# Kernel optimization log

Hardware: AMD Instinct MI355X
Metric: run time of the kernel (lower is better)

## Reference

```python
import jax, jax.numpy as jnp
import numpy as np

NUM_EXPERTS = 8
D_MODEL = 2048
D_FF = 4096
TOP_K = 2
NUM_TOKENS = 4096


def setup_inputs() -> dict:
    key = jax.random.key(0)
    k1, k2, k3, k4, k5, k6 = jax.random.split(key, 6)
    hidden_states = jax.random.normal(k1, (NUM_TOKENS, D_MODEL), dtype=jnp.float32)
    top_k_index = jax.random.randint(k2, (NUM_TOKENS, TOP_K), 0, NUM_EXPERTS)
    raw = jax.random.uniform(k3, (NUM_TOKENS, TOP_K), dtype=jnp.float32)
    top_k_weights = raw / jnp.sum(raw, axis=-1, keepdims=True)  # normalized router weights
    scale = 0.02
    Wg = jax.random.normal(k4, (NUM_EXPERTS, D_MODEL, D_FF), dtype=jnp.float32) * scale
    Wu = jax.random.normal(k5, (NUM_EXPERTS, D_MODEL, D_FF), dtype=jnp.float32) * scale
    Wd = jax.random.normal(k6, (NUM_EXPERTS, D_FF, D_MODEL), dtype=jnp.float32) * scale
    return {
        "hidden_states": hidden_states,
        "top_k_index": top_k_index,
        "top_k_weights": top_k_weights,
        "Wg": Wg,
        "Wu": Wu,
        "Wd": Wd,
    }


def reference(hidden_states, top_k_index, top_k_weights, Wg, Wu, Wd):
    T, D = hidden_states.shape
    E = Wg.shape[0]
    # Combine weights: [T, E], summing duplicate expert hits exactly as the
    # original loop's repeated index_add_ would.
    combine = jnp.zeros((T, E), dtype=top_k_weights.dtype)
    combine = combine.at[jnp.arange(T)[:, None], top_k_index].add(top_k_weights)
    # Dense all-experts SwiGLU (same math per token/expert as the gather loop)
    gate = jnp.einsum("td,edf->tef", hidden_states, Wg)   # [T, E, F]
    up = jnp.einsum("td,edf->tef", hidden_states, Wu)     # [T, E, F]
    h = jax.nn.silu(gate) * up                              # [T, E, F]
    expert_out = jnp.einsum("tef,efd->ted", h, Wd)          # [T, E, D]
    # Weighted scatter-combine
    final = jnp.einsum("ted,te->td", expert_out, combine)   # [T, D]
    return final
```

## Files before the change

kernel.cpp:

```cpp
#include <hip/hip_runtime.h>
#include <hip/hip_bf16.h>

#define NTOK 4096
#define DM   2048
#define DF   4096
#define NEXP 8
#define NPAD 10240
#define NPTILE 40

typedef __attribute__((ext_vector_type(4))) float f32x4;
typedef __attribute__((ext_vector_type(8))) short s16x8;
typedef __attribute__((ext_vector_type(2))) int   i32x2;

__device__ __forceinline__ unsigned short f2bf(float f) {
  union { float f; unsigned u; } x; x.f = f;
  unsigned r = x.u + 0x7fffu + ((x.u >> 16) & 1u);
  return (unsigned short)(r >> 16);
}
__device__ __forceinline__ unsigned pack2(float lo, float hi) {
  __hip_bfloat162 h2 = __float22bfloat162_rn(make_float2(lo, hi));
  return *reinterpret_cast<unsigned*>(&h2);
}
__device__ __forceinline__ int swz(int row, int ks) {
  return row * 32 + ((ks ^ ((row >> 1) & 3)) << 3);
}
__device__ __forceinline__ void g2l16(const void* g, void* l) {
  __builtin_amdgcn_global_load_lds(
      (const __attribute__((address_space(1))) void*)g,
      (__attribute__((address_space(3))) void*)l, 16, 0, 0);
}

#define BARRIER() asm volatile("s_barrier" ::: "memory")
#define WAITV(n)  asm volatile("s_waitcnt vmcnt(" #n ")" ::: "memory")

__global__ void k_zero_out(float* out) {
  int gid = blockIdx.x * 256 + threadIdx.x;
  *(f32x4*)(out + (size_t)gid * 4) = f32x4{0.f, 0.f, 0.f, 0.f};
}

__global__ void k_init(int* tokrow, int* counts, int* cursor) {
  int i = blockIdx.x * 256 + threadIdx.x;
  if (i < NPAD) tokrow[i] = 0;
  if (i < NEXP) { counts[i] = 0; cursor[i] = 0; }
}

__global__ void k_count(const int* __restrict__ idx, int* counts) {
  int t = blockIdx.x * 256 + threadIdx.x;
  if (t >= NTOK) return;
  int e0 = idx[2 * t], e1 = idx[2 * t + 1];
  atomicAdd(&counts[e0], 1);
  if (e1 != e0) atomicAdd(&counts[e1], 1);
}

__global__ void k_scan(const int* __restrict__ counts, int* poff) {
  if (threadIdx.x == 0) {
    int s = 0;
    for (int e = 0; e < NEXP; e++) {
      poff[e] = s;
      s += ((counts[e] + 255) & ~255);
    }
  }
}

__global__ void k_fill(const int* __restrict__ idx, const float* __restrict__ wts,
                       const int* __restrict__ poff, int* cursor,
                       int* tokrow, float* wrow) {
  int t = blockIdx.x * 256 + threadIdx.x;
  if (t >= NTOK) return;
  int e0 = idx[2 * t], e1 = idx[2 * t + 1];
  float w0 = wts[2 * t], w1 = wts[2 * t + 1];
  if (e0 == e1) {
    int g = poff[e0] + atomicAdd(&cursor[e0], 1);
    tokrow[g] = t; wrow[g] = w0 + w1;
  } else {
    int g0 = poff[e0] + atomicAdd(&cursor[e0], 1);
    tokrow[g0] = t; wrow[g0] = w0;
    int g1 = poff[e1] + atomicAdd(&cursor[e1], 1);
    tokrow[g1] = t; wrow[g1] = w1;
  }
}

__global__ void k_convX(const float* __restrict__ X, const int* __restrict__ tokrow,
                        short* __restrict__ Xg) {
  const int kt = blockIdx.x, tile = blockIdx.y, tid = threadIdx.x;
  const int part = tid & 7;
  short* dst = Xg + (size_t)(tile * 64 + kt) * 8192;
  #pragma unroll
  for (int it = 0; it < 8; it++) {
    int row = it * 32 + (tid >> 3);
    int tok = tokrow[tile * 256 + row];
    f32x4 v = *(const f32x4*)(X + (size_t)tok * DM + kt * 32 + part * 4);
    i32x2 p;
    p[0] = (int)pack2(v[0], v[1]);
    p[1] = (int)pack2(v[2], v[3]);
    int idx = row * 32 + (((part >> 1) ^ ((row >> 1) & 3)) << 3) + (part & 1) * 4;
    *(i32x2*)&dst[idx] = p;
  }
}

__global__ void k_convW(const float* __restrict__ W, short* __restrict__ dst,
                        int N, int K) {
  const int nt = blockIdx.x, kt = blockIdx.y, e = blockIdx.z;
  const int t = threadIdx.x;
  const int kg = t >> 5, nb = t & 31;
  const float* src = W + (size_t)e * K * N + (size_t)(kt * 32 + kg * 4) * N
                     + nt * 128 + nb * 4;
  f32x4 b0 = *(const f32x4*)(src);
  f32x4 b1 = *(const f32x4*)(src + N);
  f32x4 b2 = *(const f32x4*)(src + 2 * (size_t)N);
  f32x4 b3 = *(const f32x4*)(src + 3 * (size_t)N);
  short* img = dst + ((size_t)(e * (N / 128) + nt) * (K / 32) + kt) * 4096;
  const int c0 = kg >> 1, klo = (kg & 1) * 4;
  #pragma unroll
  for (int j = 0; j < 4; j++) {
    int nl = nb * 4 + j;
    i32x2 v;
    v[0] = (int)pack2(b0[j], b1[j]);
    v[1] = (int)pack2(b2[j], b3[j]);
    *(i32x2*)&img[nl * 32 + ((c0 ^ ((nl >> 1) & 3)) << 3) + klo] = v;
  }
}

__global__ __launch_bounds__(512, 2) void gemm1_kernel(
    const short* __restrict__ Xg, const short* __restrict__ Wgt,
    const short* __restrict__ Wut, const int* __restrict__ counts,
    const int* __restrict__ poff, unsigned short* __restrict__ Hs) {
  const int e = blockIdx.z;
  const int cnt = counts[e];
  const int m0 = blockIdx.y * 256;
  if (m0 >= cnt) return;
  const int nt = blockIdx.x, n0 = nt * 128;
  const int tileIdx = (poff[e] >> 8) + blockIdx.y;

  __shared__ __attribute__((aligned(16))) short As[4][8192];
  __shared__ __attribute__((aligned(16))) short Bs[4][2][4096];

  const int tid = threadIdx.x, wave = tid >> 6, lane = tid & 63;
  const int wm = wave >> 1, wn = wave & 1;
  const int lr = lane & 15, ks = lane >> 4;

  const short* aSrc = Xg + (size_t)tileIdx * 64 * 8192 + wave * 1024 + lane * 8;
  const short* gSrc = Wgt + (size_t)(e * 32 + nt) * 64 * 4096 + wave * 512 + lane * 8;
  const short* uSrc = Wut + (size_t)(e * 32 + nt) * 64 * 4096 + wave * 512 + lane * 8;

  f32x4 accg[4][4], accu[4][4];
  #pragma unroll
  for (int i = 0; i < 4; i++)
    #pragma unroll
    for (int j = 0; j < 4; j++) {
      accg[i][j] = f32x4{0.f, 0.f, 0.f, 0.f};
      accu[i][j] = f32x4{0.f, 0.f, 0.f, 0.f};
    }

  auto stage = [&](int s, int kt) {
    g2l16(aSrc + (size_t)kt * 8192,       &As[s][wave * 1024]);
    g2l16(aSrc + (size_t)kt * 8192 + 512, &As[s][wave * 1024 + 512]);
    g2l16(gSrc + (size_t)kt * 4096,       &Bs[s][0][wave * 512]);
    g2l16(uSrc + (size_t)kt * 4096,       &Bs[s][1][wave * 512]);
  };

  const int nK = DM / 32;
  stage(0, 0); stage(1, 1); stage(2, 2);
  asm volatile("s_waitcnt vmcnt(8) lgkmcnt(0)" ::: "memory");
  BARRIER();

  for (int kt = 0; kt < nK; ++kt) {
    const int s = kt & 3;
    if (kt + 3 < nK) stage((kt + 3) & 3, kt + 3);
    s16x8 af[4], bg[4], bu[4];
    #pragma unroll
    for (int mi = 0; mi < 4; mi++)
      af[mi] = *(const s16x8*)&As[s][swz(wm * 64 + mi * 16 + lr, ks)];
    #pragma unroll
    for (int ni = 0; ni < 4; ni++) {
      bg[ni] = *(const s16x8*)&Bs[s][0][swz(wn * 64 + ni * 16 + lr, ks)];
      bu[ni] = *(const s16x8*)&Bs[s][1][swz(wn * 64 + ni * 16 + lr, ks)];
    }
    __builtin_amdgcn_s_setprio(1);
    #pragma unroll
    for (int mi = 0; mi < 4; mi++)
      #pragma unroll
      for (int ni = 0; ni < 4; ni++) {
        accg[mi][ni] = __builtin_amdgcn_mfma_f32_16x16x32_bf16(af[mi], bg[ni], accg[mi][ni], 0, 0, 0);
        accu[mi][ni] = __builtin_amdgcn_mfma_f32_16x16x32_bf16(af[mi], bu[ni], accu[mi][ni], 0, 0, 0);
      }
    __builtin_amdgcn_s_setprio(0);
    if (kt + 1 < nK) {
      if (kt + 3 < nK)      { WAITV(8); }
      else if (kt + 2 < nK) { WAITV(4); }
      else                  { WAITV(0); }
      BARRIER();
    }
  }

  const size_t tb = (size_t)tileIdx * 128 * 8192;
  #pragma unroll
  for (int mi = 0; mi < 4; mi++) {
    #pragma unroll
    for (int r = 0; r < 4; r++) {
      int row = wm * 64 + mi * 16 + ks * 4 + r;
      if (m0 + row < cnt) {
        #pragma unroll
        for (int ni = 0; ni < 4; ni++) {
          int col = n0 + wn * 64 + ni * 16 + lr;
          float g = accg[mi][ni][r], u = accu[mi][ni][r];
          float sv = g / (1.f + __expf(-g));
          int ktH = col >> 5, kl = col & 31;
          Hs[tb + (size_t)ktH * 8192 + row * 32 +
             (((kl >> 3) ^ ((row >> 1) & 3)) << 3) + (kl & 7)] = f2bf(sv * u);
        }
      }
    }
  }
}

__global__ __launch_bounds__(256, 2) void gemm2_kernel(
    const unsigned short* __restrict__ Hs, const short* __restrict__ Wdt,
    const int* __restrict__ counts, const int* __restrict__ poff,
    const int* __restrict__ tokrow, const float* __restrict__ wrow,
    float* __restrict__ out) {
  const int e = blockIdx.z;
  const int cnt = counts[e];
  const int m0 = blockIdx.y * 128;
  if (m0 >= cnt) return;
  const int nt = blockIdx.x, n0 = nt * 256;
  const int tileIdx = (poff[e] >> 8) + (m0 >> 8);
  const int half = (m0 >> 7) & 1;

  __shared__ __attribute__((aligned(16))) short As[2][4096];
  __shared__ __attribute__((aligned(16))) short Bs[2][2][4096];
  __shared__ float wl[128];
  __shared__ int   tl[128];

  const int tid = threadIdx.x, wave = tid >> 6, lane = tid & 63;
  const int wm = wave >> 1, wn = wave & 1;
  const int lr = lane & 15, ks = lane >> 4;

  if (tid < 128) {
    int rp = poff[e] + m0 + tid;
    wl[tid] = wrow[rp];
    tl[tid] = tokrow[rp];
  }

  const unsigned short* aSrc = Hs + (size_t)tileIdx * 128 * 8192 + half * 4096
                               + wave * 1024 + lane * 8;
  const short* b0Src = Wdt + (size_t)(e * 16 + 2 * nt) * 128 * 4096
                       + wave * 1024 + lane * 8;
  const short* b1Src = Wdt + (size_t)(e * 16 + 2 * nt + 1) * 128 * 4096
                       + wave * 1024 + lane * 8;

  f32x4 acc0[4][4], acc1[4][4];
  #pragma unroll
  for (int i = 0; i < 4; i++)
    #pragma unroll
    for (int j = 0; j < 4; j++) {
      acc0[i][j] = f32x4{0.f, 0.f, 0.f, 0.f};
      acc1[i][j] = f32x4{0.f, 0.f, 0.f, 0.f};
    }

  auto stage = [&](int b, int kt) {
    g2l16(aSrc + (size_t)kt * 8192,        &As[b][wave * 1024]);
    g2l16(aSrc + (size_t)kt * 8192 + 512,  &As[b][wave * 1024 + 512]);
    g2l16(b0Src + (size_t)kt * 4096,       &Bs[b][0][wave * 1024]);
    g2l16(b0Src + (size_t)kt * 4096 + 512, &Bs[b][0][wave * 1024 + 512]);
    g2l16(b1Src + (size_t)kt * 4096,       &Bs[b][1][wave * 1024]);
    g2l16(b1Src + (size_t)kt * 4096 + 512, &Bs[b][1][wave * 1024 + 512]);
  };

  stage(0, 0);
  __syncthreads();
  int buf = 0;
  const int nK = DF / 32;
  for (int kt = 0; kt < nK; ++kt) {
    if (kt + 1 < nK) stage(buf ^ 1, kt + 1);
    s16x8 af[4], b0f[4], b1f[4];
    #pragma unroll
    for (int mi = 0; mi < 4; mi++)
      af[mi] = *(const s16x8*)&As[buf][swz(wm * 64 + mi * 16 + lr, ks)];
    #pragma unroll
    for (int ni = 0; ni < 4; ni++) {
      b0f[ni] = *(const s16x8*)&Bs[buf][0][swz(wn * 64 + ni * 16 + lr, ks)];
      b1f[ni] = *(const s16x8*)&Bs[buf][1][swz(wn * 64 + ni * 16 + lr, ks)];
    }
    __builtin_amdgcn_s_setprio(1);
    #pragma unroll
    for (int mi = 0; mi < 4; mi++)
      #pragma unroll
      for (int ni = 0; ni < 4; ni++) {
        acc0[mi][ni] = __builtin_amdgcn_mfma_f32_16x16x32_bf16(af[mi], b0f[ni], acc0[mi][ni], 0, 0, 0);
        acc1[mi][ni] = __builtin_amdgcn_mfma_f32_16x16x32_bf16(af[mi], b1f[ni], acc1[mi][ni], 0, 0, 0);
      }
    __builtin_amdgcn_s_setprio(0);
    __syncthreads();
    buf ^= 1;
  }

  #pragma unroll
  for (int mi = 0; mi < 4; mi++) {
    #pragma unroll
    for (int r = 0; r < 4; r++) {
      int lrow = wm * 64 + mi * 16 + ks * 4 + r;
      if (m0 + lrow < cnt) {
        float wgt = wl[lrow];
        float* obase = out + (size_t)tl[lrow] * DM + n0 + wn * 64 + lr;
        #pragma unroll
        for (int ni = 0; ni < 4; ni++) {
          atomicAdd(obase + ni * 16,       acc0[mi][ni][r] * wgt);
          atomicAdd(obase + 128 + ni * 16, acc1[mi][ni][r] * wgt);
        }
      }
    }
  }
}

extern "C" void kernel_launch(void* const* d_in, const int* in_sizes, int n_in,
                              void* d_out, int out_size, void* d_ws, size_t ws_size,
                              hipStream_t stream) {
  (void)in_sizes; (void)n_in; (void)out_size; (void)ws_size;
  const float* X   = (const float*)d_in[0];
  const int*   idx = (const int*)d_in[1];
  const float* wts = (const float*)d_in[2];
  const float* Wg  = (const float*)d_in[3];
  const float* Wu  = (const float*)d_in[4];
  const float* Wd  = (const float*)d_in[5];
  float* out = (float*)d_out;

  uint8_t* w = (uint8_t*)d_ws;
  int*   counts = (int*)(w + 0);
  int*   cursor = (int*)(w + 64);
  int*   poff   = (int*)(w + 128);
  int*   tokrow = (int*)(w + 4096);
  float* wrow   = (float*)(w + 49152);
  short* Xg     = (short*)(w + (1ull << 20));
  unsigned short* Hs = (unsigned short*)(w + (48ull << 20));
  short* Wgt    = (short*)(w + (128ull << 20));
  short* Wut    = (short*)(w + (256ull << 20));
  short* Wdt    = (short*)(w + (384ull << 20));

  k_zero_out<<<NTOK * DM / 1024, 256, 0, stream>>>(out);
  k_init<<<NPTILE, 256, 0, stream>>>(tokrow, counts, cursor);
  k_count<<<16, 256, 0, stream>>>(idx, counts);
  k_scan<<<1, 64, 0, stream>>>(counts, poff);
  k_fill<<<16, 256, 0, stream>>>(idx, wts, poff, cursor, tokrow, wrow);
  k_convX<<<dim3(DM / 32, NPTILE), 256, 0, stream>>>(X, tokrow, Xg);
  k_convW<<<dim3(DF / 128, DM / 32, NEXP), 256, 0, stream>>>(Wg, Wgt, DF, DM);
  k_convW<<<dim3(DF / 128, DM / 32, NEXP), 256, 0, stream>>>(Wu, Wut, DF, DM);
  k_convW<<<dim3(DM / 128, DF / 32, NEXP), 256, 0, stream>>>(Wd, Wdt, DM, DF);
  gemm1_kernel<<<dim3(DF / 128, 16, NEXP), 512, 0, stream>>>(Xg, Wgt, Wut, counts, poff, Hs);
  gemm2_kernel<<<dim3(DM / 256, 32, NEXP), 256, 0, stream>>>(Hs, Wdt, counts, poff, tokrow, wrow, out);
}
```

Before: 887.0 us.

## Deepen B prefetch in gate/up GEMM, register double-buffer B, remap block order

The gate/up GEMM now uses separate pipeline depths for the activation tile (3 LDS stages) and the weight tiles (5 stages). Weight fragments for the next k-step are read from LDS into registers while the current step's MFMAs run, ping-ponging between two register sets. The grid is flattened and remapped so consecutive block IDs map to different N/M tile combinations, which changes which tiles run together on CUs and may share weight tiles in L2. This costs more LDS and registers, which could reduce occupancy under the 512x2 launch bounds.

After: 911.3 us. +2.7%, slower.

```diff
diff --git a/kernel.cpp b/kernel.cpp
--- a/kernel.cpp
+++ b/kernel.cpp
@@ -126,14 +126,18 @@
     const short* __restrict__ Wut, const int* __restrict__ counts,
     const int* __restrict__ poff, unsigned short* __restrict__ Hs) {
   const int e = blockIdx.z;
+  const int lid = blockIdx.x;
+  const int logical = ((lid & 7) << 6) | (lid >> 3);
+  const int nt = logical >> 4;
+  const int yt = logical & 15;
   const int cnt = counts[e];
-  const int m0 = blockIdx.y * 256;
+  const int m0 = yt * 256;
   if (m0 >= cnt) return;
-  const int nt = blockIdx.x, n0 = nt * 128;
-  const int tileIdx = (poff[e] >> 8) + blockIdx.y;
-
-  __shared__ __attribute__((aligned(16))) short As[4][8192];
-  __shared__ __attribute__((aligned(16))) short Bs[4][2][4096];
+  const int n0 = nt * 128;
+  const int tileIdx = (poff[e] >> 8) + yt;
+
+  __shared__ __attribute__((aligned(16))) short As[3][8192];
+  __shared__ __attribute__((aligned(16))) short Bs[5][2][4096];
 
   const int tid = threadIdx.x, wave = tid >> 6, lane = tid & 63;
   const int wm = wave >> 1, wn = wave & 1;
@@ -152,46 +156,69 @@
       accu[i][j] = f32x4{0.f, 0.f, 0.f, 0.f};
     }
 
-  auto stage = [&](int s, int kt) {
+  auto stageA = [&](int s, int kt) {
     g2l16(aSrc + (size_t)kt * 8192,       &As[s][wave * 1024]);
     g2l16(aSrc + (size_t)kt * 8192 + 512, &As[s][wave * 1024 + 512]);
-    g2l16(gSrc + (size_t)kt * 4096,       &Bs[s][0][wave * 512]);
-    g2l16(uSrc + (size_t)kt * 4096,       &Bs[s][1][wave * 512]);
   };
+  auto stageB = [&](int s, int kt) {
+    g2l16(gSrc + (size_t)kt * 4096, &Bs[s][0][wave * 512]);
+    g2l16(uSrc + (size_t)kt * 4096, &Bs[s][1][wave * 512]);
+  };
 
   const int nK = DM / 32;
-  stage(0, 0); stage(1, 1); stage(2, 2);
-  asm volatile("s_waitcnt vmcnt(8) lgkmcnt(0)" ::: "memory");
+  stageB(0, 0); stageB(1, 1); stageB(2, 2); stageB(3, 3);
+  stageA(0, 0); stageA(1, 1);
+  WAITV(2);
   BARRIER();
 
-  for (int kt = 0; kt < nK; ++kt) {
-    const int s = kt & 3;
-    if (kt + 3 < nK) stage((kt + 3) & 3, kt + 3);
-    s16x8 af[4], bg[4], bu[4];
-    #pragma unroll
-    for (int mi = 0; mi < 4; mi++)
-      af[mi] = *(const s16x8*)&As[s][swz(wm * 64 + mi * 16 + lr, ks)];
-    #pragma unroll
-    for (int ni = 0; ni < 4; ni++) {
-      bg[ni] = *(const s16x8*)&Bs[s][0][swz(wn * 64 + ni * 16 + lr, ks)];
-      bu[ni] = *(const s16x8*)&Bs[s][1][swz(wn * 64 + ni * 16 + lr, ks)];
-    }
-    __builtin_amdgcn_s_setprio(1);
-    #pragma unroll
-    for (int mi = 0; mi < 4; mi++)
-      #pragma unroll
-      for (int ni = 0; ni < 4; ni++) {
-        accg[mi][ni] = __builtin_amdgcn_mfma_f32_16x16x32_bf16(af[mi], bg[ni], accg[mi][ni], 0, 0, 0);
-        accu[mi][ni] = __builtin_amdgcn_mfma_f32_16x16x32_bf16(af[mi], bu[ni], accu[mi][ni], 0, 0, 0);
-      }
-    __builtin_amdgcn_s_setprio(0);
-    if (kt + 1 < nK) {
-      if (kt + 3 < nK)      { WAITV(8); }
-      else if (kt + 2 < nK) { WAITV(4); }
-      else                  { WAITV(0); }
-      BARRIER();
-    }
-  }
+  s16x8 bgX[4], buX[4], bgY[4], buY[4];
+  #pragma unroll
+  for (int ni = 0; ni < 4; ni++) {
+    bgX[ni] = *(const s16x8*)&Bs[0][0][swz(wn * 64 + ni * 16 + lr, ks)];
+    buX[ni] = *(const s16x8*)&Bs[0][1][swz(wn * 64 + ni * 16 + lr, ks)];
+  }
+
+#define G1STEP(KT, BGC, BUC, BGN, BUN)                                         \
+  {                                                                            \
+    const int kt_ = (KT);                                                      \
+    if (kt_ + 2 < nK) stageA((kt_ + 2) % 3, kt_ + 2);                          \
+    if (kt_ + 4 < nK) stageB((kt_ + 4) % 5, kt_ + 4);                          \
+    const int sa_ = kt_ % 3;                                                   \
+    s16x8 af[4];                                                               \
+    _Pragma("unroll")                                                          \
+    for (int mi = 0; mi < 4; mi++)                                             \
+      af[mi] = *(const s16x8*)&As[sa_][swz(wm * 64 + mi * 16 + lr, ks)];       \
+    if (kt_ + 1 < nK) {                                                        \
+      const int sb_ = (kt_ + 1) % 5;                                           \
+      _Pragma("unroll")                                                        \
+      for (int ni = 0; ni < 4; ni++) {                                         \
+        BGN[ni] = *(const s16x8*)&Bs[sb_][0][swz(wn * 64 + ni * 16 + lr, ks)]; \
+        BUN[ni] = *(const s16x8*)&Bs[sb_][1][swz(wn * 64 + ni * 16 + lr, ks)]; \
+      }                                                                        \
+    }                                                                          \
+    __builtin_amdgcn_s_setprio(1);                                             \
+    _Pragma("unroll")                                                          \
+    for (int mi = 0; mi < 4; mi++)                                             \
+      _Pragma("unroll")                                                        \
+      for (int ni = 0; ni < 4; ni++) {                                         \
+        accg[mi][ni] = __builtin_amdgcn_mfma_f32_16x16x32_bf16(                \
+            af[mi], BGC[ni], accg[mi][ni], 0, 0, 0);                           \
+        accu[mi][ni] = __builtin_amdgcn_mfma_f32_16x16x32_bf16(                \
+            af[mi], BUC[ni], accu[mi][ni], 0, 0, 0);                           \
+      }                                                                        \
+    __builtin_amdgcn_s_setprio(0);                                             \
+    if (kt_ == 0)           { WAITV(4); BARRIER(); }                           \
+    else if (kt_ <= nK - 5) { WAITV(6); BARRIER(); }                           \
+    else if (kt_ == nK - 4) { WAITV(4); BARRIER(); }                           \
+    else if (kt_ == nK - 3) { WAITV(2); BARRIER(); }                           \
+    else if (kt_ == nK - 2) { WAITV(0); BARRIER(); }                           \
+  }
+
+  for (int kt = 0; kt < nK; kt += 2) {
+    G1STEP(kt,     bgX, buX, bgY, buY)
+    G1STEP(kt + 1, bgY, buY, bgX, buX)
+  }
+#undef G1STEP
 
   const size_t tb = (size_t)tileIdx * 128 * 8192;
   #pragma unroll
@@ -346,6 +373,6 @@
   k_convW<<<dim3(DF / 128, DM / 32, NEXP), 256, 0, stream>>>(Wg, Wgt, DF, DM);
   k_convW<<<dim3(DF / 128, DM / 32, NEXP), 256, 0, stream>>>(Wu, Wut, DF, DM);
   k_convW<<<dim3(DM / 128, DF / 32, NEXP), 256, 0, stream>>>(Wd, Wdt, DM, DF);
-  gemm1_kernel<<<dim3(DF / 128, 16, NEXP), 512, 0, stream>>>(Xg, Wgt, Wut, counts, poff, Hs);
+  gemm1_kernel<<<dim3(512, 1, NEXP), 512, 0, stream>>>(Xg, Wgt, Wut, counts, poff, Hs);
   gemm2_kernel<<<dim3(DM / 256, 32, NEXP), 256, 0, stream>>>(Hs, Wdt, counts, poff, tokrow, wrow, out);
 }
```

## Triple-buffer gemm2 LDS pipeline with vmcnt-based waits, drop per-row LDS tables

Applied to the files above, without the earlier changes.

The down-projection GEMM goes from a 2-stage to a 3-stage LDS ring, prefetching two K-tiles ahead. Each iteration now waits only until the next tile's loads have landed (partial vmcnt) before a barrier, instead of a full __syncthreads. The per-block token and weight tables in shared memory are removed, and the epilogue reads them straight from global memory. This raises LDS use per block, which may limit occupancy at 2 blocks per CU, and relies on the WAITV/BARRIER macros being defined earlier in the file.

Result: no change. 885.9 us (-0.1%).

```diff
diff --git a/kernel.cpp b/kernel.cpp
--- a/kernel.cpp
+++ b/kernel.cpp
@@ -226,21 +226,14 @@
   const int nt = blockIdx.x, n0 = nt * 256;
   const int tileIdx = (poff[e] >> 8) + (m0 >> 8);
   const int half = (m0 >> 7) & 1;
-
-  __shared__ __attribute__((aligned(16))) short As[2][4096];
-  __shared__ __attribute__((aligned(16))) short Bs[2][2][4096];
-  __shared__ float wl[128];
-  __shared__ int   tl[128];
+  const int roff = poff[e];
+
+  __shared__ __attribute__((aligned(16))) short As[3][4096];
+  __shared__ __attribute__((aligned(16))) short Bs[3][2][4096];
 
   const int tid = threadIdx.x, wave = tid >> 6, lane = tid & 63;
   const int wm = wave >> 1, wn = wave & 1;
   const int lr = lane & 15, ks = lane >> 4;
-
-  if (tid < 128) {
-    int rp = poff[e] + m0 + tid;
-    wl[tid] = wrow[rp];
-    tl[tid] = tokrow[rp];
-  }
 
   const unsigned short* aSrc = Hs + (size_t)tileIdx * 128 * 8192 + half * 4096
                                + wave * 1024 + lane * 8;
@@ -258,29 +251,31 @@
       acc1[i][j] = f32x4{0.f, 0.f, 0.f, 0.f};
     }
 
-  auto stage = [&](int b, int kt) {
-    g2l16(aSrc + (size_t)kt * 8192,        &As[b][wave * 1024]);
-    g2l16(aSrc + (size_t)kt * 8192 + 512,  &As[b][wave * 1024 + 512]);
-    g2l16(b0Src + (size_t)kt * 4096,       &Bs[b][0][wave * 1024]);
-    g2l16(b0Src + (size_t)kt * 4096 + 512, &Bs[b][0][wave * 1024 + 512]);
-    g2l16(b1Src + (size_t)kt * 4096,       &Bs[b][1][wave * 1024]);
-    g2l16(b1Src + (size_t)kt * 4096 + 512, &Bs[b][1][wave * 1024 + 512]);
+  auto stage = [&](int s, int kt) {
+    g2l16(aSrc + (size_t)kt * 8192,        &As[s][wave * 1024]);
+    g2l16(aSrc + (size_t)kt * 8192 + 512,  &As[s][wave * 1024 + 512]);
+    g2l16(b0Src + (size_t)kt * 4096,       &Bs[s][0][wave * 1024]);
+    g2l16(b0Src + (size_t)kt * 4096 + 512, &Bs[s][0][wave * 1024 + 512]);
+    g2l16(b1Src + (size_t)kt * 4096,       &Bs[s][1][wave * 1024]);
+    g2l16(b1Src + (size_t)kt * 4096 + 512, &Bs[s][1][wave * 1024 + 512]);
   };
 
-  stage(0, 0);
-  __syncthreads();
-  int buf = 0;
   const int nK = DF / 32;
+  stage(0, 0); stage(1, 1);
+  WAITV(6);
+  BARRIER();
+
   for (int kt = 0; kt < nK; ++kt) {
-    if (kt + 1 < nK) stage(buf ^ 1, kt + 1);
+    const int s = kt % 3;
+    if (kt + 2 < nK) stage((kt + 2) % 3, kt + 2);
     s16x8 af[4], b0f[4], b1f[4];
     #pragma unroll
     for (int mi = 0; mi < 4; mi++)
-      af[mi] = *(const s16x8*)&As[buf][swz(wm * 64 + mi * 16 + lr, ks)];
+      af[mi] = *(const s16x8*)&As[s][swz(wm * 64 + mi * 16 + lr, ks)];
     #pragma unroll
     for (int ni = 0; ni < 4; ni++) {
-      b0f[ni] = *(const s16x8*)&Bs[buf][0][swz(wn * 64 + ni * 16 + lr, ks)];
-      b1f[ni] = *(const s16x8*)&Bs[buf][1][swz(wn * 64 + ni * 16 + lr, ks)];
+      b0f[ni] = *(const s16x8*)&Bs[s][0][swz(wn * 64 + ni * 16 + lr, ks)];
+      b1f[ni] = *(const s16x8*)&Bs[s][1][swz(wn * 64 + ni * 16 + lr, ks)];
     }
     __builtin_amdgcn_s_setprio(1);
     #pragma unroll
@@ -291,8 +286,11 @@
         acc1[mi][ni] = __builtin_amdgcn_mfma_f32_16x16x32_bf16(af[mi], b1f[ni], acc1[mi][ni], 0, 0, 0);
       }
     __builtin_amdgcn_s_setprio(0);
-    __syncthreads();
-    buf ^= 1;
+    if (kt + 1 < nK) {
+      if (kt + 2 < nK) { WAITV(6); }
+      else             { WAITV(0); }
+      BARRIER();
+    }
   }
 
   #pragma unroll
@@ -301,8 +299,8 @@
     for (int r = 0; r < 4; r++) {
       int lrow = wm * 64 + mi * 16 + ks * 4 + r;
       if (m0 + lrow < cnt) {
-        float wgt = wl[lrow];
-        float* obase = out + (size_t)tl[lrow] * DM + n0 + wn * 64 + lr;
+        float wgt = wrow[roff + m0 + lrow];
+        float* obase = out + (size_t)tokrow[roff + m0 + lrow] * DM + n0 + wn * 64 + lr;
         #pragma unroll
         for (int ni = 0; ni < 4; ni++) {
           atomicAdd(obase + ni * 16,       acc0[mi][ni][r] * wgt);
```
